# Kernel tuning notes

Hardware: AMD Instinct MI355X
Metric: run time of the kernel (lower is better)

## Reference

```python
import jax, jax.numpy as jnp
import numpy as np

NEG = -65504.0  # torch.finfo(float16).min
EPS = 1e-6

B, T, D = 2, 1024, 2048
H, HD = 16, 128          # n_head, head_dim
K = 128                  # dynamic_w_hidden_dim
IH = 1                   # dynamic_hidden_dim = H // squeeze_ratio


def _rope(x, freqs_cis):
    # x: [B,T,H,hd]; 'half' mode: first/second half are the rotation pair,
    # output is interleaved (stack(...,-1).flatten(3) in torch).
    half = x.shape[-1] // 2
    a, b = x[..., :half], x[..., half:]
    cos = freqs_cis[None, :, None, :, 0]
    sin = freqs_cis[None, :, None, :, 1]
    out = jnp.stack([a * cos - b * sin, b * cos + a * sin], axis=-1)
    return out.reshape(x.shape)


def _cross_head_proj(inputs, qw1, qw2, kw1, kw2, qdd, kdd):
    # inputs: [B,N,T,S]; qw1/qw2: [B,T,I,N]; kw1/kw2: [B,S,I,N]; qdd: [B,T,N]; kdd: [B,S,N]
    out = inputs
    out = out + jnp.einsum('bnts,btin,btim->bmts', inputs, qw1, qw2)
    out = out + jnp.einsum('bnts,bsin,bsim->bmts', inputs, kw1, kw2)
    out = out + inputs * jnp.swapaxes(qdd, 1, 2)[..., None]   # [B,N,T,1]
    out = out + inputs * jnp.swapaxes(kdd, 1, 2)[:, :, None, :]  # [B,N,1,S]
    return out


def setup_inputs() -> dict:
    key = jax.random.key(0)
    ks = jax.random.split(key, 7)
    x = jax.random.normal(ks[0], (B, T, D), jnp.float32)
    mask = jnp.tril(jnp.ones((1, 1, T, T), bool))  # causal
    # rotary tables: [T, hd/2, 2] (cos, sin)
    inv = 1.0 / (10000.0 ** (jnp.arange(0, HD, 2, dtype=jnp.float32) / HD))
    ang = jnp.arange(T, dtype=jnp.float32)[:, None] * inv[None, :]
    freqs_cis = jnp.stack([jnp.cos(ang), jnp.sin(ang)], axis=-1)
    s = 0.02
    wqkv = jax.random.normal(ks[1], (D, 3 * H * HD), jnp.float32) * s
    wo = jax.random.normal(ks[2], (H * HD, D), jnp.float32) * s
    dw1 = jax.random.normal(ks[3], (D, 4, K), jnp.float32) * s
    qkw = jax.random.normal(ks[4], (4, K, 2 * IH, H), jnp.float32) * s
    dd_w = jax.random.normal(ks[5], (D, 4 * H), jnp.float32) * s
    return {"x": x, "mask": mask, "freqs_cis": freqs_cis, "wqkv": wqkv,
            "wo": wo, "dw1": dw1, "qkw": qkw, "dd_w": dd_w}


def reference(x, mask, freqs_cis, wqkv, wo, dw1, qkw, dd_w):
    b, t, d = x.shape
    qkv = x @ wqkv
    q, k, v = jnp.split(qkv, [H * HD, 2 * H * HD], axis=-1)
    q = q.reshape(b, t, H, HD)
    k = k.reshape(b, t, H, HD)
    v = v.reshape(b, t, H, HD)
    q = _rope(q, freqs_cis)
    k = _rope(k, freqs_cis)
    q = jnp.swapaxes(q, 1, 2) * (HD ** -0.5)  # [B,H,T,hd]
    k = jnp.swapaxes(k, 1, 2)
    v = jnp.swapaxes(v, 1, 2)

    # ---- DynamicWeightProjection (G=1, squeezed) ----
    dw_hidden = jax.nn.gelu(jnp.einsum('btd,dck->btck', x, dw1), approximate=False)
    w = jnp.einsum('btck,ckim->btcim', dw_hidden, qkw)  # [B,T,4,2*IH,H]
    w1, w2 = w[..., :IH, :], w[..., IH:, :]
    w1 = w1 * jax.lax.rsqrt(jnp.mean(w1 * w1, axis=-1, keepdims=True) + EPS)
    pre_qw1, pre_kw1, post_qw1, post_kw1 = [w1[:, :, i] for i in range(4)]
    pre_qw2, pre_kw2, post_qw2, post_kw2 = [w2[:, :, i] for i in range(4)]
    dd = jnp.tanh(x @ dd_w).reshape(b, t, 4, H)
    pre_qdd, pre_kdd, post_qdd, post_kdd = [dd[:, :, i] for i in range(4)]

    # ---- attention with cross-head mixing ----
    logits = jnp.einsum('bhtd,bhsd->bhts', q, k)
    logits = _cross_head_proj(logits, pre_qw1, pre_qw2, pre_kw1, pre_kw2, pre_qdd, pre_kdd)
    logits = jnp.where(mask, logits, NEG)
    probs = jax.nn.softmax(logits, axis=-1)
    probs = _cross_head_proj(probs, post_qw1, post_qw2, post_kw1, post_kw2, post_qdd, post_kdd)
    o = jnp.einsum('bhts,bhsd->bhtd', probs, v)
    o = jnp.swapaxes(o, 1, 2).reshape(b, t, H * HD)
    return o @ wo
```

## Files before the change

kernel.cpp:

```cpp
#include <hip/hip_runtime.h>


typedef unsigned short u16;
typedef unsigned int u32;
typedef __attribute__((ext_vector_type(8))) short s16x8;
typedef __attribute__((ext_vector_type(4))) float f32x4;
typedef __attribute__((ext_vector_type(2))) float f32x2;
typedef __attribute__((ext_vector_type(2))) u16 u16x2;
typedef __attribute__((ext_vector_type(8))) u16 u16x8;

#define DEV __device__ __forceinline__

DEV float bf2f(u16 u) { union { u32 u; float f; } a; a.u = ((u32)u) << 16; return a.f; }
DEV u16 f2bf(float f) {
  union { float f; u32 u; } a; a.f = f;
  u32 r = a.u + 0x7fffu + ((a.u >> 16) & 1u);
  return (u16)(r >> 16);
}

DEV void gload16(const void* g, void* l) {
  __builtin_amdgcn_global_load_lds((__attribute__((address_space(1))) void*)g,
                                   (__attribute__((address_space(3))) void*)l,
                                   16, 0, 0);
}

template <int OUTBF>
__global__ __launch_bounds__(512, 1) void gemm256(
    const u16* __restrict__ A, const u16* __restrict__ B, void* __restrict__ Cp,
    int K, int lda, int ldb, int ldc)
{
  __shared__ u16 sA[2][256 * 64];
  __shared__ u16 sB[2][256 * 64];
  const int tid = threadIdx.x, ln = tid & 63;
  const int wid = tid >> 6, wm = wid >> 2, wn = wid & 3;

  const int nx = gridDim.x;
  const int fid = blockIdx.y * nx + blockIdx.x;
  const int cpx = (nx * gridDim.y) >> 3;
  const int nid = (fid & 7) * cpx + (fid >> 3);
  const int bx = nid % nx, by = nid / nx;

  const u16* Ab = A + (size_t)(by * 256) * lda;
  const u16* Bb = B + (size_t)(bx * 256) * ldb;

  f32x4 acc[8][4];
#pragma unroll
  for (int m = 0; m < 8; ++m)
#pragma unroll
    for (int n = 0; n < 4; ++n) {
      f32x4 zz = {0.f, 0.f, 0.f, 0.f};
      acc[m][n] = zz;
    }

  int srow[4], scol[4], soff[4];
#pragma unroll
  for (int i = 0; i < 4; ++i) {
    int o = i * 8192 + tid * 16;
    soff[i] = o;
    int r = o >> 7;
    srow[i] = r;
    scol[i] = ((o & 127) ^ ((r & 7) << 4)) >> 1;
  }

#define STAGE256(ba, bb, k0)                                              \
  {                                                                       \
    _Pragma("unroll")                                                     \
    for (int i_ = 0; i_ < 4; ++i_)                                        \
      gload16(Ab + (size_t)srow[i_] * lda + (k0) + scol[i_],              \
              (char*)(ba) + soff[i_]);                                    \
    _Pragma("unroll")                                                     \
    for (int i_ = 0; i_ < 4; ++i_)                                        \
      gload16(Bb + (size_t)srow[i_] * ldb + (k0) + scol[i_],              \
              (char*)(bb) + soff[i_]);                                    \
  }

  const int arow = wm * 128 + (ln & 15);
  const int brow = wn * 64 + (ln & 15);
  const int kb = (ln >> 4) * 16;
  const int frswz = (ln & 7) << 4;
  const int NT = K >> 6;

  STAGE256(sA[0], sB[0], 0);
  asm volatile("s_waitcnt vmcnt(0)" ::: "memory");
  __builtin_amdgcn_s_barrier();

  for (int t = 0; t < NT; ++t) {
    const int c = t & 1;
    const char* pa = (const char*)sA[c];
    const char* pb = (const char*)sB[c];
    s16x8 bfr[4][2];
#pragma unroll
    for (int ph = 0; ph < 4; ++ph) {
      if (ph == 0) {
        if (t + 1 < NT) STAGE256(sA[c ^ 1], sB[c ^ 1], (t + 1) * 64);
#pragma unroll
        for (int n = 0; n < 4; ++n)
#pragma unroll
          for (int kk = 0; kk < 2; ++kk)
            bfr[n][kk] = *(const s16x8*)(pb + (size_t)(brow + n * 16) * 128 + ((kk * 64 + kb) ^ frswz));
      }
      s16x8 afr[2][2];
#pragma unroll
      for (int mm = 0; mm < 2; ++mm)
#pragma unroll
        for (int kk = 0; kk < 2; ++kk)
          afr[mm][kk] = *(const s16x8*)(pa + (size_t)(arow + (ph * 2 + mm) * 16) * 128 + ((kk * 64 + kb) ^ frswz));
      __builtin_amdgcn_s_barrier();
      __builtin_amdgcn_s_setprio(1);
#pragma unroll
      for (int mm = 0; mm < 2; ++mm)
#pragma unroll
        for (int n = 0; n < 4; ++n)
#pragma unroll
          for (int kk = 0; kk < 2; ++kk)
            acc[ph * 2 + mm][n] = __builtin_amdgcn_mfma_f32_16x16x32_bf16(
                afr[mm][kk], bfr[n][kk], acc[ph * 2 + mm][n], 0, 0, 0);
      __builtin_amdgcn_s_setprio(0);
    }
    asm volatile("s_waitcnt vmcnt(0)" ::: "memory");
    __builtin_amdgcn_s_barrier();
  }
#undef STAGE256

  const int r0 = by * 256 + wm * 128 + ((ln >> 4) << 2);
  const int c0 = bx * 256 + wn * 64 + (ln & 15);
#pragma unroll
  for (int m = 0; m < 8; ++m)
#pragma unroll
    for (int n = 0; n < 4; ++n)
#pragma unroll
      for (int j = 0; j < 4; ++j) {
        int row = r0 + m * 16 + j, col = c0 + n * 16;
        if (OUTBF)
          ((u16*)Cp)[(size_t)row * ldc + col] = f2bf(acc[m][n][j]);
        else
          ((float*)Cp)[(size_t)row * ldc + col] = acc[m][n][j];
      }
}

template <int OUTBF>
__global__ __launch_bounds__(256) void gemm_bt(
    const u16* __restrict__ A, const u16* __restrict__ B, void* __restrict__ Cp,
    int K, int lda, int ldb, int ldc,
    long sAb, long sBb, long sCb1, long sCb2, int CZ2, int cmode, int swz)
{
  int bx = blockIdx.x, by = blockIdx.y;
  if (swz) {
    int nx = gridDim.x;
    int fid = by * nx + bx;
    int cpx = (nx * gridDim.y) >> 3;
    int nid = (fid & 7) * cpx + (fid >> 3);
    bx = nid % nx; by = nid / nx;
  }
  if (cmode == 1 && bx > by) return;
  __shared__ u16 sA[128 * 64];
  __shared__ u16 sB[128 * 64];
  const int tid = threadIdx.x, wv = tid >> 6, ln = tid & 63;
  const int z = blockIdx.z;
  const u16* Ab = A + (size_t)z * sAb + (size_t)(by * 128) * lda;
  const u16* Bb = B + (size_t)z * sBb + (size_t)(bx * 128) * ldb;
  const int wr = (wv >> 1) * 64, wc = (wv & 1) * 64;
  const int Keff = (cmode == 2) ? min(K, (by + 1) * 128) : K;

  f32x4 acc[4][4];
#pragma unroll
  for (int m = 0; m < 4; ++m)
#pragma unroll
    for (int n = 0; n < 4; ++n) {
      f32x4 zz = {0.f, 0.f, 0.f, 0.f};
      acc[m][n] = zz;
    }

  int o_[4], r_[4], cb_[4];
#pragma unroll
  for (int i = 0; i < 4; ++i) {
    int o = (wv * 4 + i) * 1024 + ln * 16;
    o_[i] = o;
    int r = o >> 7;
    r_[i] = r;
    cb_[i] = (o & 127) ^ ((r & 7) << 4);
  }
  const int frswz = (ln & 7) << 4;
  const int fkcol = (ln >> 4) << 4;

  for (int k0 = 0; k0 < Keff; k0 += 64) {
    __syncthreads();
#pragma unroll
    for (int i = 0; i < 4; ++i)
      gload16(Ab + (size_t)r_[i] * lda + (k0 + (cb_[i] >> 1)), (char*)sA + o_[i]);
#pragma unroll
    for (int i = 0; i < 4; ++i)
      gload16(Bb + (size_t)r_[i] * ldb + (k0 + (cb_[i] >> 1)), (char*)sB + o_[i]);
    __syncthreads();

#pragma unroll
    for (int ks = 0; ks < 2; ++ks) {
      s16x8 av[4], bv[4];
#pragma unroll
      for (int m = 0; m < 4; ++m) {
        int row = wr + m * 16 + (ln & 15);
        int addr = row * 128 + ((ks * 64 + fkcol) ^ frswz);
        av[m] = *(const s16x8*)((const char*)sA + addr);
      }
#pragma unroll
      for (int n = 0; n < 4; ++n) {
        int row = wc + n * 16 + (ln & 15);
        int addr = row * 128 + ((ks * 64 + fkcol) ^ frswz);
        bv[n] = *(const s16x8*)((const char*)sB + addr);
      }
#pragma unroll
      for (int m = 0; m < 4; ++m)
#pragma unroll
        for (int n = 0; n < 4; ++n)
          acc[m][n] = __builtin_amdgcn_mfma_f32_16x16x32_bf16(av[m], bv[n], acc[m][n], 0, 0, 0);
    }
  }

  const size_t cbase = (size_t)(z / CZ2) * sCb1 + (size_t)(z % CZ2) * sCb2;
  const int r0 = by * 128 + wr + ((ln >> 4) << 2);
  const int c0 = bx * 128 + wc + (ln & 15);
#pragma unroll
  for (int m = 0; m < 4; ++m)
#pragma unroll
    for (int n = 0; n < 4; ++n)
#pragma unroll
      for (int j = 0; j < 4; ++j) {
        int row = r0 + m * 16 + j, col = c0 + n * 16;
        if (OUTBF)
          ((u16*)Cp)[cbase + (size_t)row * ldc + col] = f2bf(acc[m][n][j]);
        else
          ((float*)Cp)[cbase + (size_t)row * ldc + col] = acc[m][n][j];
      }
}

template <int INBF>
__global__ __launch_bounds__(256) void transpose_to_bf16(
    const void* __restrict__ srcv, u16* __restrict__ dst,
    int R, int C, int Cpad, int srcLd, long sSrc1, long sSrc2, int Z2, long sDst)
{
  __shared__ float tile[32][33];
  const int z = blockIdx.z, z1 = z / Z2, z2 = z % Z2;
  const size_t sbase = (size_t)z1 * sSrc1 + (size_t)z2 * sSrc2;
  u16* d = dst + (size_t)z * sDst;
  const int c0 = blockIdx.x * 32, r0 = blockIdx.y * 32;
  const int tx = threadIdx.x, ty = threadIdx.y;
#pragma unroll
  for (int i = 0; i < 4; ++i) {
    int r = r0 + ty + i * 8, c = c0 + tx;
    float v = 0.f;
    if (c < C && r < R) {
      if (INBF) v = bf2f(((const u16*)srcv)[sbase + (size_t)r * srcLd + c]);
      else      v = ((const float*)srcv)[sbase + (size_t)r * srcLd + c];
    }
    tile[ty + i * 8][tx] = v;
  }
  __syncthreads();
#pragma unroll
  for (int i = 0; i < 4; ++i) {
    int dr = c0 + ty + i * 8, dc = r0 + tx;
    if (dr < Cpad && dc < R) d[(size_t)dr * R + dc] = f2bf(tile[tx][ty + i * 8]);
  }
}

__global__ void cvt_f32_bf16_k(const float* __restrict__ src, u16* __restrict__ dst, int n4) {
  int i = blockIdx.x * 256 + threadIdx.x;
  if (i >= n4) return;
  const float4 v = ((const float4*)src)[i];
  u16* o = dst + (size_t)i * 4;
  o[0] = f2bf(v.x); o[1] = f2bf(v.y); o[2] = f2bf(v.z); o[3] = f2bf(v.w);
}

__global__ __launch_bounds__(256) void rope_k(
    const u16* __restrict__ qkvm, const float* __restrict__ fc,
    u16* __restrict__ qb, u16* __restrict__ kb)
{
  const int bt = blockIdx.x, b = bt >> 10, t = bt & 1023;
  const u16* row = qkvm + (size_t)bt * 6912;
  const float SC = 0.08838834764831845f;
#pragma unroll
  for (int it = 0; it < 4; ++it) {
    int idx = threadIdx.x + it * 256;
    int h = idx >> 6, j = idx & 63;
    float c = fc[(t * 64 + j) * 2], sn = fc[(t * 64 + j) * 2 + 1];
    float qa = bf2f(row[h * 128 + j]), qbv = bf2f(row[h * 128 + 64 + j]);
    float ka = bf2f(row[2048 + h * 128 + j]), kbv = bf2f(row[2048 + h * 128 + 64 + j]);
    size_t o = ((size_t)(b * 16 + h) * 1024 + t) * 128 + 2 * j;
    qb[o]     = f2bf((qa * c - qbv * sn) * SC);
    qb[o + 1] = f2bf((qbv * c + qa * sn) * SC);
    kb[o]     = f2bf(ka * c - kbv * sn);
    kb[o + 1] = f2bf(kbv * c + ka * sn);
  }
}

__global__ __launch_bounds__(64) void gelu_bf16_k(u16* __restrict__ qm) {
  int bt = blockIdx.x, tid = threadIdx.x;
  u16* p = qm + (size_t)bt * 6912 + 6144 + tid * 8;
  u16x8 v = *(u16x8*)p;
#pragma unroll
  for (int i = 0; i < 8; ++i) {
    float f = bf2f(v[i]);
    f = 0.5f * f * (1.f + erff(f * 0.70710678118654752f));
    v[i] = f2bf(f);
  }
  *(u16x8*)p = v;
}

__global__ __launch_bounds__(64) void wproj_k(
    const u16* __restrict__ qkvm, const float* __restrict__ qkw,
    float* __restrict__ w1a, float* __restrict__ w2a, float* __restrict__ kpT)
{
  const int bt = blockIdx.x, ln = threadIdx.x;
  const int c = ln >> 4, m = ln & 15;
  const int b = bt >> 10, t = bt & 1023;
  const u16* hp = qkvm + (size_t)bt * 6912 + 6144 + c * 128;
  const float* Wp = qkw + (size_t)c * 4096 + m;
  float w1 = 0.f, w2 = 0.f;
  for (int k = 0; k < 128; ++k) {
    float hv = bf2f(hp[k]);
    w1 += hv * Wp[k * 32];
    w2 += hv * Wp[k * 32 + 16];
  }
  float ss = w1 * w1;
  ss += __shfl_xor(ss, 1); ss += __shfl_xor(ss, 2);
  ss += __shfl_xor(ss, 4); ss += __shfl_xor(ss, 8);
  float nrm = rsqrtf(ss * (1.f / 16.f) + 1e-6f);
  float w1n = w1 * nrm;
  size_t o = (size_t)bt * 64 + c * 16 + m;
  w1a[o] = w1n;
  w2a[o] = w2;
  size_t kb = (size_t)b * 98304 + (size_t)m * 1024 + t;
  if (c == 1) { kpT[kb] = w1n; kpT[kb + 16384] = w2; }
  if (c == 3) { kpT[kb + 49152] = w1n; kpT[kb + 65536] = w2; }
}

__global__ __launch_bounds__(64) void dd_k(const u16* __restrict__ qkvm,
                                           float* __restrict__ dda, float* __restrict__ kpT) {
  int bt = blockIdx.x, ln = threadIdx.x;
  int c = ln >> 4, m = ln & 15;
  int b = bt >> 10, t = bt & 1023;
  float v = tanhf(bf2f(qkvm[(size_t)bt * 6912 + 6656 + ln]));
  dda[(size_t)bt * 64 + ln] = v;
  size_t kb = (size_t)b * 98304 + (size_t)m * 1024 + t;
  if (c == 1) kpT[kb + 32768] = v;
  if (c == 3) kpT[kb + 81920] = v;
}

__global__ __launch_bounds__(512, 2) void proj_softmax_k(
    const float* __restrict__ L, u16* __restrict__ P,
    const float* __restrict__ w1a, const float* __restrict__ w2a,
    const float* __restrict__ dda, const float* __restrict__ kparT)
{
  const int t0 = blockIdx.x * 2, b = blockIdx.y;
  const int tid = threadIdx.x, wv = tid >> 6, ln = tid & 63;
  const int s0 = tid * 2;
  const bool liveB = (s0 <= t0 + 1);

  __shared__ float qpar[2][6][16];
  __shared__ float red2[2][16][8];
  __shared__ float rzf[2][16];
  if (tid < 192) {
    int tt = (tid >= 96) ? 1 : 0, u = tid - tt * 96;
    int a = u >> 4, hh = u & 15;
    const float* sp = (a == 0 || a == 3) ? w1a : ((a == 1 || a == 4) ? w2a : dda);
    int cc = (a < 3) ? 0 : 2;
    qpar[tt][a][hh] = sp[(size_t)(b * 1024 + t0 + tt) * 64 + cc * 16 + hh];
  }
  __syncthreads();

  const float* kp = kparT + (size_t)b * 98304 + s0;
  float vA[16][2], vB[16][2];
  const size_t lbaseA = ((size_t)(b * 16) * 1024 + t0) * 1024 + s0;
  const size_t lbaseB = lbaseA + 1024;

  if (liveB) {
#pragma unroll
    for (int h = 0; h < 16; ++h) {
      f32x2 dA = *(const f32x2*)(L + lbaseA + (size_t)h * 1048576);
      f32x2 dB = *(const f32x2*)(L + lbaseB + (size_t)h * 1048576);
      vA[h][0] = dA[0]; vA[h][1] = dA[1];
      vB[h][0] = dB[0]; vB[h][1] = dB[1];
    }
    float dqA0 = 0.f, dqA1 = 0.f, dkA0 = 0.f, dkA1 = 0.f;
    float dqB0 = 0.f, dqB1 = 0.f, dkB0 = 0.f, dkB1 = 0.f;
#pragma unroll
    for (int h = 0; h < 16; ++h) {
      f32x2 k1 = *(const f32x2*)(kp + h * 1024);
      dqA0 += vA[h][0] * qpar[0][0][h]; dqA1 += vA[h][1] * qpar[0][0][h];
      dkA0 += vA[h][0] * k1[0];         dkA1 += vA[h][1] * k1[1];
      dqB0 += vB[h][0] * qpar[1][0][h]; dqB1 += vB[h][1] * qpar[1][0][h];
      dkB0 += vB[h][0] * k1[0];         dkB1 += vB[h][1] * k1[1];
    }
    const bool okA0 = (s0 <= t0), okA1 = (s0 + 1 <= t0), okB1 = (s0 + 1 <= t0 + 1);
#pragma unroll
    for (int h = 0; h < 16; ++h) {
      f32x2 k2 = *(const f32x2*)(kp + 16384 + h * 1024);
      f32x2 kd = *(const f32x2*)(kp + 32768 + h * 1024);
      float aA0 = vA[h][0] * (1.f + qpar[0][2][h] + kd[0]) + qpar[0][1][h] * dqA0 + k2[0] * dkA0;
      float aA1 = vA[h][1] * (1.f + qpar[0][2][h] + kd[1]) + qpar[0][1][h] * dqA1 + k2[1] * dkA1;
      float aB0 = vB[h][0] * (1.f + qpar[1][2][h] + kd[0]) + qpar[1][1][h] * dqB0 + k2[0] * dkB0;
      float aB1 = vB[h][1] * (1.f + qpar[1][2][h] + kd[1]) + qpar[1][1][h] * dqB1 + k2[1] * dkB1;
      vA[h][0] = okA0 ? __expf(aA0) : 0.f;
      vA[h][1] = okA1 ? __expf(aA1) : 0.f;
      vB[h][0] = __expf(aB0);
      vB[h][1] = okB1 ? __expf(aB1) : 0.f;
    }
  } else {
#pragma unroll
    for (int h = 0; h < 16; ++h) {
      vA[h][0] = 0.f; vA[h][1] = 0.f; vB[h][0] = 0.f; vB[h][1] = 0.f;
    }
  }

#pragma unroll
  for (int h = 0; h < 16; ++h) {
    float xA = vA[h][0] + vA[h][1];
    float xB = vB[h][0] + vB[h][1];
#pragma unroll
    for (int off = 32; off > 0; off >>= 1) {
      xA += __shfl_xor(xA, off);
      xB += __shfl_xor(xB, off);
    }
    if (ln == 0) { red2[0][h][wv] = xA; red2[1][h][wv] = xB; }
  }
  __syncthreads();
  if (tid < 32) {
    int tt = tid >> 4, h = tid & 15;
    rzf[tt][h] = 1.f / (((red2[tt][h][0] + red2[tt][h][1]) + (red2[tt][h][2] + red2[tt][h][3])) +
                        ((red2[tt][h][4] + red2[tt][h][5]) + (red2[tt][h][6] + red2[tt][h][7])));
  }
  __syncthreads();

  const size_t pbaseA = lbaseA, pbaseB = lbaseB;
  if (liveB) {
    float pdqA0 = 0.f, pdqA1 = 0.f, pdkA0 = 0.f, pdkA1 = 0.f;
    float pdqB0 = 0.f, pdqB1 = 0.f, pdkB0 = 0.f, pdkB1 = 0.f;
#pragma unroll
    for (int h = 0; h < 16; ++h) {
      f32x2 k1 = *(const f32x2*)(kp + 49152 + h * 1024);
      float rzA = rzf[0][h], rzB = rzf[1][h];
      float pA0 = vA[h][0] * rzA, pA1 = vA[h][1] * rzA;
      float pB0 = vB[h][0] * rzB, pB1 = vB[h][1] * rzB;
      vA[h][0] = pA0; vA[h][1] = pA1; vB[h][0] = pB0; vB[h][1] = pB1;
      pdqA0 += pA0 * qpar[0][3][h]; pdqA1 += pA1 * qpar[0][3][h];
      pdkA0 += pA0 * k1[0];         pdkA1 += pA1 * k1[1];
      pdqB0 += pB0 * qpar[1][3][h]; pdqB1 += pB1 * qpar[1][3][h];
      pdkB0 += pB0 * k1[0];         pdkB1 += pB1 * k1[1];
    }
#pragma unroll
    for (int h = 0; h < 16; ++h) {
      f32x2 k2 = *(const f32x2*)(kp + 65536 + h * 1024);
      f32x2 kd = *(const f32x2*)(kp + 81920 + h * 1024);
      u16x2 pkA, pkB;
      pkA[0] = f2bf(vA[h][0] * (1.f + qpar[0][5][h] + kd[0]) + qpar[0][4][h] * pdqA0 + k2[0] * pdkA0);
      pkA[1] = f2bf(vA[h][1] * (1.f + qpar[0][5][h] + kd[1]) + qpar[0][4][h] * pdqA1 + k2[1] * pdkA1);
      pkB[0] = f2bf(vB[h][0] * (1.f + qpar[1][5][h] + kd[0]) + qpar[1][4][h] * pdqB0 + k2[0] * pdkB0);
      pkB[1] = f2bf(vB[h][1] * (1.f + qpar[1][5][h] + kd[1]) + qpar[1][4][h] * pdqB1 + k2[1] * pdkB1);
      *(u16x2*)(P + pbaseA + (size_t)h * 1048576) = pkA;
      *(u16x2*)(P + pbaseB + (size_t)h * 1048576) = pkB;
    }
  } else {
    u16x2 z2 = {0, 0};
#pragma unroll
    for (int h = 0; h < 16; ++h) {
      *(u16x2*)(P + pbaseA + (size_t)h * 1048576) = z2;
      *(u16x2*)(P + pbaseB + (size_t)h * 1048576) = z2;
    }
  }
}

extern "C" void kernel_launch(void* const* d_in, const int* in_sizes, int n_in,
                              void* d_out, int out_size, void* d_ws, size_t ws_size,
                              hipStream_t stream)
{
  (void)in_sizes; (void)n_in; (void)out_size; (void)ws_size;
  const float* x    = (const float*)d_in[0];
  const float* fc   = (const float*)d_in[2];
  const float* wqkv = (const float*)d_in[3];
  const float* wo   = (const float*)d_in[4];
  const float* dw1  = (const float*)d_in[5];
  const float* qkw  = (const float*)d_in[6];
  const float* ddw  = (const float*)d_in[7];
  float* out = (float*)d_out;
  char* w = (char*)d_ws;

  u16*   woT   = (u16*)(w + 0);
  u16*   qb    = (u16*)(w + 8388608);
  u16*   kb    = (u16*)(w + 16777216);
  u16*   vT    = (u16*)(w + 25165824);
  u16*   obf   = (u16*)(w + 33554432);
  float* w1a   = (float*)(w + 41943040);
  float* w2a   = (float*)(w + 42467328);
  float* dda   = (float*)(w + 42991616);
  const size_t TB = 43515904;
  u16*   xb    = (u16*)(w + TB);
  u16*   wallT = (u16*)(w + TB + 8388608);
  u16*   qkvm  = (u16*)(w + TB + 36700160);
  float* L     = (float*)(w + TB);
  u16*   P     = (u16*)(w + TB + 134217728);
  float* kparT = (float*)(w + 244842496);

  cvt_f32_bf16_k<<<4096, 256, 0, stream>>>(x, xb, 1048576);
  transpose_to_bf16<0><<<dim3(192, 64, 1), dim3(32, 8), 0, stream>>>(wqkv, wallT, 2048, 6144, 6144, 6144, 0, 0, 1, 0);
  transpose_to_bf16<0><<<dim3(16, 64, 1),  dim3(32, 8), 0, stream>>>(dw1,  wallT + (size_t)6144 * 2048, 2048, 512, 512, 512, 0, 0, 1, 0);
  transpose_to_bf16<0><<<dim3(8, 64, 1),   dim3(32, 8), 0, stream>>>(ddw,  wallT + (size_t)6656 * 2048, 2048, 64, 256, 64, 0, 0, 1, 0);
  transpose_to_bf16<0><<<dim3(64, 64, 1),  dim3(32, 8), 0, stream>>>(wo,   woT, 2048, 2048, 2048, 2048, 0, 0, 1, 0);

  gemm256<1><<<dim3(27, 8, 1), 512, 0, stream>>>(xb, wallT, qkvm, 2048, 2048, 2048, 6912);
  rope_k<<<2048, 256, 0, stream>>>(qkvm, fc, qb, kb);
  transpose_to_bf16<1><<<dim3(4, 32, 32), dim3(32, 8), 0, stream>>>(qkvm + 4096, vT, 1024, 128, 128, 6912, 7077888, 128, 16, 131072);

  gelu_bf16_k<<<2048, 64, 0, stream>>>(qkvm);
  wproj_k<<<2048, 64, 0, stream>>>(qkvm, qkw, w1a, w2a, kparT);
  dd_k<<<2048, 64, 0, stream>>>(qkvm, dda, kparT);

  gemm_bt<0><<<dim3(8, 8, 32), 256, 0, stream>>>(qb, kb, L, 128, 128, 128, 1024, 131072, 131072, 1048576, 0, 1, 1, 0);
  proj_softmax_k<<<dim3(512, 2, 1), 512, 0, stream>>>(L, P, w1a, w2a, dda, kparT);
  gemm_bt<1><<<dim3(1, 8, 32), 256, 0, stream>>>(P, vT, obf, 1024, 1024, 1024, 2048, 1048576, 131072, 2097152, 128, 16, 2, 0);

  gemm_bt<0><<<dim3(16, 16, 1), 256, 0, stream>>>(obf, woT, out, 2048, 2048, 2048, 2048, 0, 0, 0, 0, 1, 0, 1);
}
```

Measured before the change: 317.7 us.

## Prefetch two K-tiles ahead in gemm256 and split softmax rows per block

The gemm256 main loop now issues loads for tile t+2 right after finishing compute on buffer c, and waits with a partial vmcnt count instead of draining all loads. This keeps two stages of global-to-LDS loads in flight, so load latency overlaps better with MFMA work. Separately, proj_softmax_k handles one query row per block instead of two, doubling the grid and raising launch bounds to 4 blocks per CU. That cuts register pressure and aims for higher occupancy, at the cost of loading the k-side parameters twice as often.

```diff
diff --git a/kernel.cpp b/kernel.cpp
--- a/kernel.cpp
+++ b/kernel.cpp
@@ -81,18 +81,18 @@
   const int NT = K >> 6;
 
   STAGE256(sA[0], sB[0], 0);
-  asm volatile("s_waitcnt vmcnt(0)" ::: "memory");
-  __builtin_amdgcn_s_barrier();
+  if (NT > 1) STAGE256(sA[1], sB[1], 64);
 
   for (int t = 0; t < NT; ++t) {
     const int c = t & 1;
+    asm volatile("s_waitcnt vmcnt(8)" ::: "memory");
+    __builtin_amdgcn_s_barrier();
     const char* pa = (const char*)sA[c];
     const char* pb = (const char*)sB[c];
     s16x8 bfr[4][2];
 #pragma unroll
     for (int ph = 0; ph < 4; ++ph) {
       if (ph == 0) {
-        if (t + 1 < NT) STAGE256(sA[c ^ 1], sB[c ^ 1], (t + 1) * 64);
 #pragma unroll
         for (int n = 0; n < 4; ++n)
 #pragma unroll
@@ -117,8 +117,8 @@
                 afr[mm][kk], bfr[n][kk], acc[ph * 2 + mm][n], 0, 0, 0);
       __builtin_amdgcn_s_setprio(0);
     }
-    asm volatile("s_waitcnt vmcnt(0)" ::: "memory");
     __builtin_amdgcn_s_barrier();
+    if (t + 2 < NT) STAGE256(sA[c], sB[c], (t + 2) * 64);
   }
 #undef STAGE256
 
@@ -345,126 +345,95 @@
   if (c == 3) kpT[kb + 81920] = v;
 }
 
-__global__ __launch_bounds__(512, 2) void proj_softmax_k(
+__global__ __launch_bounds__(512, 4) void proj_softmax_k(
     const float* __restrict__ L, u16* __restrict__ P,
     const float* __restrict__ w1a, const float* __restrict__ w2a,
     const float* __restrict__ dda, const float* __restrict__ kparT)
 {
-  const int t0 = blockIdx.x * 2, b = blockIdx.y;
+  const int t = blockIdx.x, b = blockIdx.y;
   const int tid = threadIdx.x, wv = tid >> 6, ln = tid & 63;
   const int s0 = tid * 2;
-  const bool liveB = (s0 <= t0 + 1);
-
-  __shared__ float qpar[2][6][16];
-  __shared__ float red2[2][16][8];
-  __shared__ float rzf[2][16];
-  if (tid < 192) {
-    int tt = (tid >= 96) ? 1 : 0, u = tid - tt * 96;
-    int a = u >> 4, hh = u & 15;
+  const bool live = (s0 <= t);
+
+  __shared__ float qpar[6][16];
+  __shared__ float red2[16][8];
+  __shared__ float rzf[16];
+  if (tid < 96) {
+    int a = tid >> 4, hh = tid & 15;
     const float* sp = (a == 0 || a == 3) ? w1a : ((a == 1 || a == 4) ? w2a : dda);
     int cc = (a < 3) ? 0 : 2;
-    qpar[tt][a][hh] = sp[(size_t)(b * 1024 + t0 + tt) * 64 + cc * 16 + hh];
+    qpar[a][hh] = sp[(size_t)(b * 1024 + t) * 64 + cc * 16 + hh];
   }
   __syncthreads();
 
   const float* kp = kparT + (size_t)b * 98304 + s0;
-  float vA[16][2], vB[16][2];
-  const size_t lbaseA = ((size_t)(b * 16) * 1024 + t0) * 1024 + s0;
-  const size_t lbaseB = lbaseA + 1024;
-
-  if (liveB) {
+  float v[16][2];
+  const size_t lbase = ((size_t)(b * 16) * 1024 + t) * 1024 + s0;
+
+  if (live) {
 #pragma unroll
     for (int h = 0; h < 16; ++h) {
-      f32x2 dA = *(const f32x2*)(L + lbaseA + (size_t)h * 1048576);
-      f32x2 dB = *(const f32x2*)(L + lbaseB + (size_t)h * 1048576);
-      vA[h][0] = dA[0]; vA[h][1] = dA[1];
-      vB[h][0] = dB[0]; vB[h][1] = dB[1];
-    }
-    float dqA0 = 0.f, dqA1 = 0.f, dkA0 = 0.f, dkA1 = 0.f;
-    float dqB0 = 0.f, dqB1 = 0.f, dkB0 = 0.f, dkB1 = 0.f;
+      f32x2 d = *(const f32x2*)(L + lbase + (size_t)h * 1048576);
+      v[h][0] = d[0]; v[h][1] = d[1];
+    }
+    float dq0 = 0.f, dq1 = 0.f, dk0 = 0.f, dk1 = 0.f;
 #pragma unroll
     for (int h = 0; h < 16; ++h) {
       f32x2 k1 = *(const f32x2*)(kp + h * 1024);
-      dqA0 += vA[h][0] * qpar[0][0][h]; dqA1 += vA[h][1] * qpar[0][0][h];
-      dkA0 += vA[h][0] * k1[0];         dkA1 += vA[h][1] * k1[1];
-      dqB0 += vB[h][0] * qpar[1][0][h]; dqB1 += vB[h][1] * qpar[1][0][h];
-      dkB0 += vB[h][0] * k1[0];         dkB1 += vB[h][1] * k1[1];
-    }
-    const bool okA0 = (s0 <= t0), okA1 = (s0 + 1 <= t0), okB1 = (s0 + 1 <= t0 + 1);
+      dq0 += v[h][0] * qpar[0][h]; dq1 += v[h][1] * qpar[0][h];
+      dk0 += v[h][0] * k1[0];      dk1 += v[h][1] * k1[1];
+    }
+    const bool ok1 = (s0 + 1 <= t);
 #pragma unroll
     for (int h = 0; h < 16; ++h) {
       f32x2 k2 = *(const f32x2*)(kp + 16384 + h * 1024);
       f32x2 kd = *(const f32x2*)(kp + 32768 + h * 1024);
-      float aA0 = vA[h][0] * (1.f + qpar[0][2][h] + kd[0]) + qpar[0][1][h] * dqA0 + k2[0] * dkA0;
-      float aA1 = vA[h][1] * (1.f + qpar[0][2][h] + kd[1]) + qpar[0][1][h] * dqA1 + k2[1] * dkA1;
-      float aB0 = vB[h][0] * (1.f + qpar[1][2][h] + kd[0]) + qpar[1][1][h] * dqB0 + k2[0] * dkB0;
-      float aB1 = vB[h][1] * (1.f + qpar[1][2][h] + kd[1]) + qpar[1][1][h] * dqB1 + k2[1] * dkB1;
-      vA[h][0] = okA0 ? __expf(aA0) : 0.f;
-      vA[h][1] = okA1 ? __expf(aA1) : 0.f;
-      vB[h][0] = __expf(aB0);
-      vB[h][1] = okB1 ? __expf(aB1) : 0.f;
-    }
-  } else {
+      float a0 = v[h][0] * (1.f + qpar[2][h] + kd[0]) + qpar[1][h] * dq0 + k2[0] * dk0;
+      float a1 = v[h][1] * (1.f + qpar[2][h] + kd[1]) + qpar[1][h] * dq1 + k2[1] * dk1;
+      v[h][0] = __expf(a0);
+      v[h][1] = ok1 ? __expf(a1) : 0.f;
+    }
+  }
+
+#pragma unroll
+  for (int h = 0; h < 16; ++h) {
+    float x = live ? (v[h][0] + v[h][1]) : 0.f;
+#pragma unroll
+    for (int off = 32; off > 0; off >>= 1) x += __shfl_xor(x, off);
+    if (ln == 0) red2[h][wv] = x;
+  }
+  __syncthreads();
+  if (tid < 16)
+    rzf[tid] = 1.f / (((red2[tid][0] + red2[tid][1]) + (red2[tid][2] + red2[tid][3])) +
+                      ((red2[tid][4] + red2[tid][5]) + (red2[tid][6] + red2[tid][7])));
+  __syncthreads();
+
+  const size_t pbase = ((size_t)(b * 16) * 1024 + t) * 1024 + s0;
+  if (live) {
+    float pdq0 = 0.f, pdq1 = 0.f, pdk0 = 0.f, pdk1 = 0.f;
 #pragma unroll
     for (int h = 0; h < 16; ++h) {
-      vA[h][0] = 0.f; vA[h][1] = 0.f; vB[h][0] = 0.f; vB[h][1] = 0.f;
-    }
-  }
-
-#pragma unroll
-  for (int h = 0; h < 16; ++h) {
-    float xA = vA[h][0] + vA[h][1];
-    float xB = vB[h][0] + vB[h][1];
-#pragma unroll
-    for (int off = 32; off > 0; off >>= 1) {
-      xA += __shfl_xor(xA, off);
-      xB += __shfl_xor(xB, off);
-    }
-    if (ln == 0) { red2[0][h][wv] = xA; red2[1][h][wv] = xB; }
-  }
-  __syncthreads();
-  if (tid < 32) {
-    int tt = tid >> 4, h = tid & 15;
-    rzf[tt][h] = 1.f / (((red2[tt][h][0] + red2[tt][h][1]) + (red2[tt][h][2] + red2[tt][h][3])) +
-                        ((red2[tt][h][4] + red2[tt][h][5]) + (red2[tt][h][6] + red2[tt][h][7])));
-  }
-  __syncthreads();
-
-  const size_t pbaseA = lbaseA, pbaseB = lbaseB;
-  if (liveB) {
-    float pdqA0 = 0.f, pdqA1 = 0.f, pdkA0 = 0.f, pdkA1 = 0.f;
-    float pdqB0 = 0.f, pdqB1 = 0.f, pdkB0 = 0.f, pdkB1 = 0.f;
-#pragma unroll
-    for (int h = 0; h < 16; ++h) {
+      float rz = rzf[h];
       f32x2 k1 = *(const f32x2*)(kp + 49152 + h * 1024);
-      float rzA = rzf[0][h], rzB = rzf[1][h];
-      float pA0 = vA[h][0] * rzA, pA1 = vA[h][1] * rzA;
-      float pB0 = vB[h][0] * rzB, pB1 = vB[h][1] * rzB;
-      vA[h][0] = pA0; vA[h][1] = pA1; vB[h][0] = pB0; vB[h][1] = pB1;
-      pdqA0 += pA0 * qpar[0][3][h]; pdqA1 += pA1 * qpar[0][3][h];
-      pdkA0 += pA0 * k1[0];         pdkA1 += pA1 * k1[1];
-      pdqB0 += pB0 * qpar[1][3][h]; pdqB1 += pB1 * qpar[1][3][h];
-      pdkB0 += pB0 * k1[0];         pdkB1 += pB1 * k1[1];
+      float p0 = v[h][0] * rz, p1 = v[h][1] * rz;
+      v[h][0] = p0; v[h][1] = p1;
+      pdq0 += p0 * qpar[3][h]; pdq1 += p1 * qpar[3][h];
+      pdk0 += p0 * k1[0];      pdk1 += p1 * k1[1];
     }
 #pragma unroll
     for (int h = 0; h < 16; ++h) {
       f32x2 k2 = *(const f32x2*)(kp + 65536 + h * 1024);
       f32x2 kd = *(const f32x2*)(kp + 81920 + h * 1024);
-      u16x2 pkA, pkB;
-      pkA[0] = f2bf(vA[h][0] * (1.f + qpar[0][5][h] + kd[0]) + qpar[0][4][h] * pdqA0 + k2[0] * pdkA0);
-      pkA[1] = f2bf(vA[h][1] * (1.f + qpar[0][5][h] + kd[1]) + qpar[0][4][h] * pdqA1 + k2[1] * pdkA1);
-      pkB[0] = f2bf(vB[h][0] * (1.f + qpar[1][5][h] + kd[0]) + qpar[1][4][h] * pdqB0 + k2[0] * pdkB0);
-      pkB[1] = f2bf(vB[h][1] * (1.f + qpar[1][5][h] + kd[1]) + qpar[1][4][h] * pdqB1 + k2[1] * pdkB1);
-      *(u16x2*)(P + pbaseA + (size_t)h * 1048576) = pkA;
-      *(u16x2*)(P + pbaseB + (size_t)h * 1048576) = pkB;
+      u16x2 pk;
+      pk[0] = f2bf(v[h][0] * (1.f + qpar[5][h] + kd[0]) + qpar[4][h] * pdq0 + k2[0] * pdk0);
+      pk[1] = f2bf(v[h][1] * (1.f + qpar[5][h] + kd[1]) + qpar[4][h] * pdq1 + k2[1] * pdk1);
+      *(u16x2*)(P + pbase + (size_t)h * 1048576) = pk;
     }
   } else {
     u16x2 z2 = {0, 0};
 #pragma unroll
-    for (int h = 0; h < 16; ++h) {
-      *(u16x2*)(P + pbaseA + (size_t)h * 1048576) = z2;
-      *(u16x2*)(P + pbaseB + (size_t)h * 1048576) = z2;
-    }
+    for (int h = 0; h < 16; ++h)
+      *(u16x2*)(P + pbase + (size_t)h * 1048576) = z2;
   }
 }
 
@@ -514,7 +483,7 @@
   dd_k<<<2048, 64, 0, stream>>>(qkvm, dda, kparT);
 
   gemm_bt<0><<<dim3(8, 8, 32), 256, 0, stream>>>(qb, kb, L, 128, 128, 128, 1024, 131072, 131072, 1048576, 0, 1, 1, 0);
-  proj_softmax_k<<<dim3(512, 2, 1), 512, 0, stream>>>(L, P, w1a, w2a, dda, kparT);
+  proj_softmax_k<<<dim3(1024, 2, 1), 512, 0, stream>>>(L, P, w1a, w2a, dda, kparT);
   gemm_bt<1><<<dim3(1, 8, 32), 256, 0, stream>>>(P, vT, obf, 1024, 1024, 1024, 2048, 1048576, 131072, 2097152, 128, 16, 2, 0);
 
   gemm_bt<0><<<dim3(16, 16, 1), 256, 0, stream>>>(obf, woT, out, 2048, 2048, 2048, 2048, 0, 0, 0, 0, 1, 0, 1);
```

New measurement: 318.6 us. No clear change (+0.3%).
